# Performance work log

Hardware: AMD Instinct MI355X
Metric: run time of the kernel (lower is better)

## Reference

```python
import jax, jax.numpy as jnp
import numpy as np

B, LQ, LK, D = 8, 2048, 2048, 128

def setup_inputs() -> dict:
    key = jax.random.key(0)
    k1, k2, k3, k4 = jax.random.split(key, 4)
    return {
        "query": jax.random.normal(k1, (B, LQ, D), dtype=jnp.float32),
        "key": jax.random.normal(k2, (B, LK, D), dtype=jnp.float32),
        "value": jax.random.normal(k3, (B, LK, D), dtype=jnp.float32),
        "scale_factor": jax.random.normal(k4, (B, LQ, LK), dtype=jnp.float32),
    }

def reference(query, key, value, scale_factor):
    # qk: [B, LQ, LK]
    qk = jnp.einsum("bqd,bkd->bqk", query, key)
    probs = jax.nn.softmax(qk * scale_factor, axis=-1)
    # dropout_p = 0.0 -> identity
    return jnp.einsum("bqk,bkd->bqd", probs, value)
```

## Files before the change

kernel.cpp:

```cpp
#include <hip/hip_runtime.h>
#include <hip/hip_bf16.h>


typedef float          f32x4 __attribute__((ext_vector_type(4)));
typedef short          s16x8 __attribute__((ext_vector_type(8)));
typedef unsigned int   u32x4 __attribute__((ext_vector_type(4)));
typedef unsigned short u16x4 __attribute__((ext_vector_type(4)));

#define LOG2E 1.4426950408889634f

__device__ __forceinline__ float fast_exp2(float x) {
#if __has_builtin(__builtin_amdgcn_exp2f)
    return __builtin_amdgcn_exp2f(x);
#else
    return exp2f(x);
#endif
}

__device__ __forceinline__ unsigned short f2bf(float x) {
    return __builtin_bit_cast(unsigned short, __float2bfloat16(x));
}
__device__ __forceinline__ float bf2f(unsigned short u) {
    return __bfloat162float(__builtin_bit_cast(__hip_bfloat16, u));
}

__global__ void conv_split(const float* __restrict__ src,
                           unsigned short* __restrict__ hi,
                           unsigned short* __restrict__ lo, int n4) {
    int i = blockIdx.x * blockDim.x + threadIdx.x;
    if (i >= n4) return;
    const float4 v = ((const float4*)src)[i];
    float f[4] = {v.x, v.y, v.z, v.w};
    u16x4 h, l;
#pragma unroll
    for (int j = 0; j < 4; ++j) {
        unsigned short hb = f2bf(f[j]);
        h[j] = hb;
        l[j] = f2bf(f[j] - bf2f(hb));
    }
    ((u16x4*)hi)[i] = h;
    ((u16x4*)lo)[i] = l;
}

__global__ void transpose_v(const float* __restrict__ v,
                            unsigned short* __restrict__ vt) {
    __shared__ unsigned short tile[64 * 132];
    const int b   = blockIdx.x & 7;
    const int k0  = (blockIdx.x >> 3) * 64;
    const int tid = threadIdx.x;
#pragma unroll
    for (int p = 0; p < 8; ++p) {
        int idx  = p * 256 + tid;
        int k    = idx >> 5;
        int dblk = idx & 31;
        float4 val = ((const float4*)v)[((b * 2048 + k0 + k) * 128 + dblk * 4) >> 2];
        u16x4 t4;
        t4[0] = f2bf(val.x); t4[1] = f2bf(val.y);
        t4[2] = f2bf(val.z); t4[3] = f2bf(val.w);
        *(u16x4*)&tile[k * 132 + dblk * 4] = t4;
    }
    __syncthreads();
#pragma unroll
    for (int p = 0; p < 4; ++p) {
        int idx = p * 256 + tid;
        int d   = idx >> 3;
        int k8  = idx & 7;
        u16x4 a, c;
#pragma unroll
        for (int j = 0; j < 4; ++j) a[j] = tile[(k8 * 8 + j) * 132 + d];
#pragma unroll
        for (int j = 0; j < 4; ++j) c[j] = tile[(k8 * 8 + 4 + j) * 132 + d];
        unsigned short* outp = vt + (b * 128 + d) * 2048 + k0 + k8 * 8;
        *(u16x4*)outp       = a;
        *(u16x4*)(outp + 4) = c;
    }
}

#define KHS 136
#define VTS 72
#define PS  72

__global__ __launch_bounds__(256, 2)
void flash_fwd(const unsigned short* __restrict__ qh_g,
               const unsigned short* __restrict__ ql_g,
               const unsigned short* __restrict__ kh_g,
               const unsigned short* __restrict__ kl_g,
               const unsigned short* __restrict__ vt_g,
               const float* __restrict__ scale_g,
               float* __restrict__ opart,
               float* __restrict__ mpart,
               float* __restrict__ lpart) {
    __shared__ unsigned short lds_kh[64 * KHS];
    __shared__ unsigned short lds_kl[64 * KHS];
    __shared__ unsigned short lds_vt[128 * VTS];
    __shared__ unsigned short lds_p[4][16 * PS];

    const int tid  = threadIdx.x;
    const int wave = tid >> 6;
    const int lane = tid & 63;
    const int c    = lane & 15;
    const int g    = lane >> 4;

    const int bid   = blockIdx.x;
    const int b     = bid & 7;
    const int qt    = (bid >> 3) & 31;
    const int ks    = bid >> 8;
    const int q0    = qt * 64;
    const int kbase = ks * 1024;

    s16x8 qh[4], ql[4];
    {
        const int qrow = b * 2048 + q0 + wave * 16 + c;
#pragma unroll
        for (int kstep = 0; kstep < 4; ++kstep) {
            int idx = qrow * 16 + kstep * 4 + g;
            qh[kstep] = __builtin_bit_cast(s16x8, ((const u32x4*)qh_g)[idx]);
            ql[kstep] = __builtin_bit_cast(s16x8, ((const u32x4*)ql_g)[idx]);
        }
    }

    f32x4 oacc[8];
#pragma unroll
    for (int t = 0; t < 8; ++t) oacc[t] = (f32x4){0.f, 0.f, 0.f, 0.f};
    float m2[4], ln[4];
#pragma unroll
    for (int r = 0; r < 4; ++r) { m2[r] = -INFINITY; ln[r] = 0.f; }

    for (int kc = 0; kc < 16; ++kc) {
        const int k0 = kbase + kc * 64;

        __syncthreads();
        {
            u32x4 tk[4], tl[4], tv[4];
            const int row = tid >> 4, c8 = tid & 15;
            const int dv  = tid >> 3, k8 = tid & 7;
#pragma unroll
            for (int p = 0; p < 4; ++p) {
                int gidx = (b * 2048 + k0 + p * 16 + row) * 16 + c8;
                tk[p] = ((const u32x4*)kh_g)[gidx];
                tl[p] = ((const u32x4*)kl_g)[gidx];
                int vidx = (b * 128 + p * 32 + dv) * 256 + (k0 >> 3) + k8;
                tv[p] = ((const u32x4*)vt_g)[vidx];
            }
#pragma unroll
            for (int p = 0; p < 4; ++p) {
                *(u32x4*)&lds_kh[(p * 16 + row) * KHS + c8 * 8] = tk[p];
                *(u32x4*)&lds_kl[(p * 16 + row) * KHS + c8 * 8] = tl[p];
                *(u32x4*)&lds_vt[(p * 32 + dv) * VTS + k8 * 8]  = tv[p];
            }
        }
        __syncthreads();

        float sc[4][4];
        {
            const int qrow = b * 2048 + q0 + wave * 16 + g * 4;
#pragma unroll
            for (int r = 0; r < 4; ++r)
#pragma unroll
                for (int t = 0; t < 4; ++t)
                    sc[t][r] = scale_g[(qrow + r) * 2048 + k0 + t * 16 + c] * LOG2E;
        }

        f32x4 s[4];
#pragma unroll
        for (int t = 0; t < 4; ++t) s[t] = (f32x4){0.f, 0.f, 0.f, 0.f};
#pragma unroll
        for (int kstep = 0; kstep < 4; ++kstep) {
#pragma unroll
            for (int t = 0; t < 4; ++t) {
                int off = (t * 16 + c) * KHS + kstep * 32 + g * 8;
                s16x8 bh = *(const s16x8*)&lds_kh[off];
                s16x8 bl = *(const s16x8*)&lds_kl[off];
                s[t] = __builtin_amdgcn_mfma_f32_16x16x32_bf16(qh[kstep], bh, s[t], 0, 0, 0);
                s[t] = __builtin_amdgcn_mfma_f32_16x16x32_bf16(ql[kstep], bh, s[t], 0, 0, 0);
                s[t] = __builtin_amdgcn_mfma_f32_16x16x32_bf16(qh[kstep], bl, s[t], 0, 0, 0);
            }
        }

        float lt[4][4], mx[4];
#pragma unroll
        for (int r = 0; r < 4; ++r) {
            lt[0][r] = s[0][r] * sc[0][r];
            lt[1][r] = s[1][r] * sc[1][r];
            lt[2][r] = s[2][r] * sc[2][r];
            lt[3][r] = s[3][r] * sc[3][r];
            mx[r] = fmaxf(fmaxf(lt[0][r], lt[1][r]), fmaxf(lt[2][r], lt[3][r]));
        }
#pragma unroll
        for (int mask = 1; mask < 16; mask <<= 1)
#pragma unroll
            for (int r = 0; r < 4; ++r)
                mx[r] = fmaxf(mx[r], __shfl_xor(mx[r], mask));
        float al[4], rs[4];
#pragma unroll
        for (int r = 0; r < 4; ++r) {
            float mn = fmaxf(m2[r], mx[r]);
            al[r] = fast_exp2(m2[r] - mn);
            m2[r] = mn;
            rs[r] = 0.f;
        }
#pragma unroll
        for (int t = 0; t < 4; ++t)
#pragma unroll
            for (int r = 0; r < 4; ++r) {
                float p = fast_exp2(lt[t][r] - m2[r]);
                rs[r] += p;
                lds_p[wave][(g * 4 + r) * PS + t * 16 + c] = f2bf(p);
            }
#pragma unroll
        for (int mask = 1; mask < 16; mask <<= 1)
#pragma unroll
            for (int r = 0; r < 4; ++r)
                rs[r] += __shfl_xor(rs[r], mask);
#pragma unroll
        for (int r = 0; r < 4; ++r) ln[r] = ln[r] * al[r] + rs[r];
#pragma unroll
        for (int t = 0; t < 8; ++t)
#pragma unroll
            for (int r = 0; r < 4; ++r) oacc[t][r] *= al[r];

#pragma unroll
        for (int k2 = 0; k2 < 2; ++k2) {
            s16x8 af = *(const s16x8*)&lds_p[wave][c * PS + k2 * 32 + g * 8];
#pragma unroll
            for (int t2 = 0; t2 < 8; ++t2) {
                s16x8 bv = *(const s16x8*)&lds_vt[(t2 * 16 + c) * VTS + k2 * 32 + g * 8];
                oacc[t2] = __builtin_amdgcn_mfma_f32_16x16x32_bf16(af, bv, oacc[t2], 0, 0, 0);
            }
        }
    }

    {
        const int rowb = (ks * 8 + b) * 2048 + q0 + wave * 16;
#pragma unroll
        for (int t2 = 0; t2 < 8; ++t2)
#pragma unroll
            for (int r = 0; r < 4; ++r)
                opart[(rowb + g * 4 + r) * 128 + t2 * 16 + c] = oacc[t2][r];
        if (c == 0) {
#pragma unroll
            for (int r = 0; r < 4; ++r) {
                mpart[rowb + g * 4 + r] = m2[r];
                lpart[rowb + g * 4 + r] = ln[r];
            }
        }
    }
}

__global__ void merge_halves(const float* __restrict__ opart,
                             const float* __restrict__ mpart,
                             const float* __restrict__ lpart,
                             float* __restrict__ out) {
    const int row = blockIdx.x;
    const int d   = threadIdx.x;
    const float m0 = mpart[row],  m1 = mpart[16384 + row];
    const float l0 = lpart[row],  l1 = lpart[16384 + row];
    const float M  = fmaxf(m0, m1);
    const float a0 = fast_exp2(m0 - M);
    const float a1 = fast_exp2(m1 - M);
    const float inv = 1.f / (a0 * l0 + a1 * l1);
    const int i = row * 128 + d;
    out[i] = (a0 * opart[i] + a1 * opart[16384 * 128 + i]) * inv;
}

extern "C" void kernel_launch(void* const* d_in, const int* in_sizes, int n_in,
                              void* d_out, int out_size, void* d_ws, size_t ws_size,
                              hipStream_t stream) {
    const float* q  = (const float*)d_in[0];
    const float* k  = (const float*)d_in[1];
    const float* v  = (const float*)d_in[2];
    const float* sc = (const float*)d_in[3];
    float* out = (float*)d_out;

    char* ws = (char*)d_ws;
    const size_t MB = 1024 * 1024;
    unsigned short* qh = (unsigned short*)(ws);
    unsigned short* ql = (unsigned short*)(ws + 4 * MB);
    unsigned short* kh = (unsigned short*)(ws + 8 * MB);
    unsigned short* kl = (unsigned short*)(ws + 12 * MB);
    unsigned short* vt = (unsigned short*)(ws + 16 * MB);
    float* opart = (float*)(ws + 20 * MB);
    float* mpart = (float*)(ws + 36 * MB);
    float* lpart = (float*)(ws + 36 * MB + 128 * 1024);

    conv_split<<<2048, 256, 0, stream>>>(q, qh, ql, 524288);
    conv_split<<<2048, 256, 0, stream>>>(k, kh, kl, 524288);
    transpose_v<<<256, 256, 0, stream>>>(v, vt);
    flash_fwd<<<512, 256, 0, stream>>>(qh, ql, kh, kl, vt, sc, opart, mpart, lpart);
    merge_halves<<<16384, 128, 0, stream>>>(opart, mpart, lpart, out);
}
```

Measured before the change: 260.3 us.

## Split keys four ways, load K/V from global directly, bf16 partial outputs

Rewrites the attention kernel to split the key dimension into four chunks instead of two, doubling the grid and raising the occupancy target. K and V are read straight from global memory into MFMA fragments with register prefetch, which removes the LDS staging and block barriers. S is computed transposed so each lane reads the scale factors as vectorized rows, and the P tile is stored with an XOR swizzle. Partial outputs are stored in bf16, which cuts merge traffic at some cost in precision. The Q and K conversion kernels are fused into one launch, and the V transpose gets smaller tiles.

```diff
diff --git a/kernel.cpp b/kernel.cpp
--- a/kernel.cpp
+++ b/kernel.cpp
@@ -16,7 +16,6 @@
     return exp2f(x);
 #endif
 }
-
 __device__ __forceinline__ unsigned short f2bf(float x) {
     return __builtin_bit_cast(unsigned short, __float2bfloat16(x));
 }
@@ -24,11 +23,15 @@
     return __bfloat162float(__builtin_bit_cast(__hip_bfloat16, u));
 }
 
-__global__ void conv_split(const float* __restrict__ src,
-                           unsigned short* __restrict__ hi,
-                           unsigned short* __restrict__ lo, int n4) {
-    int i = blockIdx.x * blockDim.x + threadIdx.x;
-    if (i >= n4) return;
+__global__ void conv_split2(const float* __restrict__ q, const float* __restrict__ k,
+                            unsigned short* __restrict__ qh, unsigned short* __restrict__ ql,
+                            unsigned short* __restrict__ kh, unsigned short* __restrict__ kl) {
+    const int bid  = blockIdx.x;
+    const int half = bid >> 11;
+    const int i    = (bid & 2047) * 256 + threadIdx.x;
+    const float* src = half ? k : q;
+    unsigned short* hi = half ? kh : qh;
+    unsigned short* lo = half ? kl : ql;
     const float4 v = ((const float4*)src)[i];
     float f[4] = {v.x, v.y, v.z, v.w};
     u16x4 h, l;
@@ -44,223 +47,200 @@
 
 __global__ void transpose_v(const float* __restrict__ v,
                             unsigned short* __restrict__ vt) {
-    __shared__ unsigned short tile[64 * 132];
-    const int b   = blockIdx.x & 7;
-    const int k0  = (blockIdx.x >> 3) * 64;
-    const int tid = threadIdx.x;
-#pragma unroll
-    for (int p = 0; p < 8; ++p) {
-        int idx  = p * 256 + tid;
-        int k    = idx >> 5;
-        int dblk = idx & 31;
-        float4 val = ((const float4*)v)[((b * 2048 + k0 + k) * 128 + dblk * 4) >> 2];
+    __shared__ unsigned short tile[64 * 36];
+    const int b    = blockIdx.x & 7;
+    const int rest = blockIdx.x >> 3;
+    const int k0   = (rest & 31) * 64;
+    const int d0   = (rest >> 5) * 32;
+    const int tid  = threadIdx.x;
+#pragma unroll
+    for (int it = 0; it < 2; ++it) {
+        int idx = it * 256 + tid;
+        int kk  = idx >> 3;
+        int d4  = idx & 7;
+        float4 val = ((const float4*)v)[((b * 2048 + k0 + kk) * 128 + d0 + d4 * 4) >> 2];
         u16x4 t4;
         t4[0] = f2bf(val.x); t4[1] = f2bf(val.y);
         t4[2] = f2bf(val.z); t4[3] = f2bf(val.w);
-        *(u16x4*)&tile[k * 132 + dblk * 4] = t4;
+        *(u16x4*)&tile[kk * 36 + d4 * 4] = t4;
     }
     __syncthreads();
-#pragma unroll
-    for (int p = 0; p < 4; ++p) {
-        int idx = p * 256 + tid;
-        int d   = idx >> 3;
-        int k8  = idx & 7;
-        u16x4 a, c;
-#pragma unroll
-        for (int j = 0; j < 4; ++j) a[j] = tile[(k8 * 8 + j) * 132 + d];
-#pragma unroll
-        for (int j = 0; j < 4; ++j) c[j] = tile[(k8 * 8 + 4 + j) * 132 + d];
-        unsigned short* outp = vt + (b * 128 + d) * 2048 + k0 + k8 * 8;
+    {
+        int d  = tid >> 3;
+        int k8 = tid & 7;
+        u16x4 a, cgrp;
+#pragma unroll
+        for (int j = 0; j < 4; ++j) a[j]    = tile[(k8 * 8 + j) * 36 + d];
+#pragma unroll
+        for (int j = 0; j < 4; ++j) cgrp[j] = tile[(k8 * 8 + 4 + j) * 36 + d];
+        unsigned short* outp = vt + (b * 128 + d0 + d) * 2048 + k0 + k8 * 8;
         *(u16x4*)outp       = a;
-        *(u16x4*)(outp + 4) = c;
-    }
-}
-
-#define KHS 136
-#define VTS 72
-#define PS  72
-
-__global__ __launch_bounds__(256, 2)
+        *(u16x4*)(outp + 4) = cgrp;
+    }
+}
+
+#define KSPLIT 4
+#define NKC    8
+
+__global__ __launch_bounds__(256, 4)
 void flash_fwd(const unsigned short* __restrict__ qh_g,
                const unsigned short* __restrict__ ql_g,
                const unsigned short* __restrict__ kh_g,
                const unsigned short* __restrict__ kl_g,
                const unsigned short* __restrict__ vt_g,
                const float* __restrict__ scale_g,
-               float* __restrict__ opart,
+               unsigned short* __restrict__ opart,
                float* __restrict__ mpart,
                float* __restrict__ lpart) {
-    __shared__ unsigned short lds_kh[64 * KHS];
-    __shared__ unsigned short lds_kl[64 * KHS];
-    __shared__ unsigned short lds_vt[128 * VTS];
-    __shared__ unsigned short lds_p[4][16 * PS];
+    __shared__ unsigned short lds_p[4][16 * 72];
 
     const int tid  = threadIdx.x;
     const int wave = tid >> 6;
     const int lane = tid & 63;
     const int c    = lane & 15;
     const int g    = lane >> 4;
-
-    const int bid   = blockIdx.x;
-    const int b     = bid & 7;
-    const int qt    = (bid >> 3) & 31;
-    const int ks    = bid >> 8;
-    const int q0    = qt * 64;
-    const int kbase = ks * 1024;
-
-    s16x8 qh[4], ql[4];
+    const int xr   = (c & 3) << 3;
+
+    const int bid = blockIdx.x;
+    const int b   = bid & 7;
+    const int qt  = (bid >> 3) & 31;
+    const int ks  = bid >> 8;
+    const int q0  = qt * 64;
+    const int kbase = ks * 512;
+
+    const int qrow = b * 2048 + q0 + wave * 16 + c;
+
+    s16x8 qhB[4], qlB[4];
+#pragma unroll
+    for (int kstep = 0; kstep < 4; ++kstep) {
+        int idx = qrow * 16 + kstep * 4 + g;
+        qhB[kstep] = __builtin_bit_cast(s16x8, ((const u32x4*)qh_g)[idx]);
+        qlB[kstep] = __builtin_bit_cast(s16x8, ((const u32x4*)ql_g)[idx]);
+    }
+
+    f32x4 oacc[8];
+#pragma unroll
+    for (int t = 0; t < 8; ++t) oacc[t] = (f32x4){0.f, 0.f, 0.f, 0.f};
+    float m2 = -INFINITY, ln = 0.f;
+    unsigned short* pw = &lds_p[wave][0];
+
+    for (int kc = 0; kc < NKC; ++kc) {
+        const int k0 = kbase + kc * 64;
+
+        f32x4 scf[4];
+        {
+            const int sidx = qrow * 512 + (k0 >> 2) + g;
+#pragma unroll
+            for (int t = 0; t < 4; ++t)
+                scf[t] = ((const f32x4*)scale_g)[sidx + 4 * t];
+        }
+
+        f32x4 st[4];
+#pragma unroll
+        for (int t = 0; t < 4; ++t) st[t] = (f32x4){0.f, 0.f, 0.f, 0.f};
+        {
+            const u32x4* khp = (const u32x4*)kh_g + ((b * 2048 + k0 + c) * 16 + g);
+            const u32x4* klp = (const u32x4*)kl_g + ((b * 2048 + k0 + c) * 16 + g);
+            s16x8 khf = __builtin_bit_cast(s16x8, khp[0]);
+            s16x8 klf = __builtin_bit_cast(s16x8, klp[0]);
+#pragma unroll
+            for (int p = 0; p < 16; ++p) {
+                const int t = p & 3, kstep = p >> 2;
+                s16x8 khn, kln;
+                if (p < 15) {
+                    const int off = ((p + 1) & 3) * 256 + ((p + 1) >> 2) * 4;
+                    khn = __builtin_bit_cast(s16x8, khp[off]);
+                    kln = __builtin_bit_cast(s16x8, klp[off]);
+                }
+                st[t] = __builtin_amdgcn_mfma_f32_16x16x32_bf16(khf, qhB[kstep], st[t], 0, 0, 0);
+                st[t] = __builtin_amdgcn_mfma_f32_16x16x32_bf16(klf, qhB[kstep], st[t], 0, 0, 0);
+                st[t] = __builtin_amdgcn_mfma_f32_16x16x32_bf16(khf, qlB[kstep], st[t], 0, 0, 0);
+                if (p < 15) { khf = khn; klf = kln; }
+            }
+        }
+
+        float lt[4][4];
+        float mx = -INFINITY;
+#pragma unroll
+        for (int t = 0; t < 4; ++t)
+#pragma unroll
+            for (int r = 0; r < 4; ++r) {
+                lt[t][r] = st[t][r] * (scf[t][r] * LOG2E);
+                mx = fmaxf(mx, lt[t][r]);
+            }
+        mx = fmaxf(mx, __shfl_xor(mx, 16));
+        mx = fmaxf(mx, __shfl_xor(mx, 32));
+        const float mn = fmaxf(m2, mx);
+        const float al = fast_exp2(m2 - mn);
+        m2 = mn;
+        float rs = 0.f;
+#pragma unroll
+        for (int t = 0; t < 4; ++t) {
+            u16x4 pb;
+#pragma unroll
+            for (int r = 0; r < 4; ++r) {
+                float pv = fast_exp2(lt[t][r] - m2);
+                rs += pv;
+                pb[r] = f2bf(pv);
+            }
+            *(u16x4*)&pw[c * 72 + (((16 * t + 4 * g) ^ xr))] = pb;
+        }
+        rs += __shfl_xor(rs, 16);
+        rs += __shfl_xor(rs, 32);
+        ln = ln * al + rs;
+#pragma unroll
+        for (int t2 = 0; t2 < 8; ++t2)
+#pragma unroll
+            for (int r = 0; r < 4; ++r) oacc[t2][r] *= al;
+
+        {
+            const u32x4* vp = (const u32x4*)vt_g + ((b * 128 + c) * 256 + (k0 >> 3) + g);
+#pragma unroll
+            for (int k2 = 0; k2 < 2; ++k2) {
+                s16x8 bP = *(const s16x8*)&pw[c * 72 + ((32 * k2 + 8 * g) ^ xr)];
+#pragma unroll
+                for (int t2 = 0; t2 < 8; ++t2) {
+                    s16x8 vA = __builtin_bit_cast(s16x8, vp[t2 * (16 * 256) + 4 * k2]);
+                    oacc[t2] = __builtin_amdgcn_mfma_f32_16x16x32_bf16(vA, bP, oacc[t2], 0, 0, 0);
+                }
+            }
+        }
+    }
+
     {
-        const int qrow = b * 2048 + q0 + wave * 16 + c;
-#pragma unroll
-        for (int kstep = 0; kstep < 4; ++kstep) {
-            int idx = qrow * 16 + kstep * 4 + g;
-            qh[kstep] = __builtin_bit_cast(s16x8, ((const u32x4*)qh_g)[idx]);
-            ql[kstep] = __builtin_bit_cast(s16x8, ((const u32x4*)ql_g)[idx]);
-        }
-    }
-
-    f32x4 oacc[8];
-#pragma unroll
-    for (int t = 0; t < 8; ++t) oacc[t] = (f32x4){0.f, 0.f, 0.f, 0.f};
-    float m2[4], ln[4];
-#pragma unroll
-    for (int r = 0; r < 4; ++r) { m2[r] = -INFINITY; ln[r] = 0.f; }
-
-    for (int kc = 0; kc < 16; ++kc) {
-        const int k0 = kbase + kc * 64;
-
-        __syncthreads();
-        {
-            u32x4 tk[4], tl[4], tv[4];
-            const int row = tid >> 4, c8 = tid & 15;
-            const int dv  = tid >> 3, k8 = tid & 7;
-#pragma unroll
-            for (int p = 0; p < 4; ++p) {
-                int gidx = (b * 2048 + k0 + p * 16 + row) * 16 + c8;
-                tk[p] = ((const u32x4*)kh_g)[gidx];
-                tl[p] = ((const u32x4*)kl_g)[gidx];
-                int vidx = (b * 128 + p * 32 + dv) * 256 + (k0 >> 3) + k8;
-                tv[p] = ((const u32x4*)vt_g)[vidx];
-            }
-#pragma unroll
-            for (int p = 0; p < 4; ++p) {
-                *(u32x4*)&lds_kh[(p * 16 + row) * KHS + c8 * 8] = tk[p];
-                *(u32x4*)&lds_kl[(p * 16 + row) * KHS + c8 * 8] = tl[p];
-                *(u32x4*)&lds_vt[(p * 32 + dv) * VTS + k8 * 8]  = tv[p];
-            }
-        }
-        __syncthreads();
-
-        float sc[4][4];
-        {
-            const int qrow = b * 2048 + q0 + wave * 16 + g * 4;
-#pragma unroll
-            for (int r = 0; r < 4; ++r)
-#pragma unroll
-                for (int t = 0; t < 4; ++t)
-                    sc[t][r] = scale_g[(qrow + r) * 2048 + k0 + t * 16 + c] * LOG2E;
-        }
-
-        f32x4 s[4];
-#pragma unroll
-        for (int t = 0; t < 4; ++t) s[t] = (f32x4){0.f, 0.f, 0.f, 0.f};
-#pragma unroll
-        for (int kstep = 0; kstep < 4; ++kstep) {
-#pragma unroll
-            for (int t = 0; t < 4; ++t) {
-                int off = (t * 16 + c) * KHS + kstep * 32 + g * 8;
-                s16x8 bh = *(const s16x8*)&lds_kh[off];
-                s16x8 bl = *(const s16x8*)&lds_kl[off];
-                s[t] = __builtin_amdgcn_mfma_f32_16x16x32_bf16(qh[kstep], bh, s[t], 0, 0, 0);
-                s[t] = __builtin_amdgcn_mfma_f32_16x16x32_bf16(ql[kstep], bh, s[t], 0, 0, 0);
-                s[t] = __builtin_amdgcn_mfma_f32_16x16x32_bf16(qh[kstep], bl, s[t], 0, 0, 0);
-            }
-        }
-
-        float lt[4][4], mx[4];
-#pragma unroll
-        for (int r = 0; r < 4; ++r) {
-            lt[0][r] = s[0][r] * sc[0][r];
-            lt[1][r] = s[1][r] * sc[1][r];
-            lt[2][r] = s[2][r] * sc[2][r];
-            lt[3][r] = s[3][r] * sc[3][r];
-            mx[r] = fmaxf(fmaxf(lt[0][r], lt[1][r]), fmaxf(lt[2][r], lt[3][r]));
-        }
-#pragma unroll
-        for (int mask = 1; mask < 16; mask <<= 1)
-#pragma unroll
-            for (int r = 0; r < 4; ++r)
-                mx[r] = fmaxf(mx[r], __shfl_xor(mx[r], mask));
-        float al[4], rs[4];
-#pragma unroll
-        for (int r = 0; r < 4; ++r) {
-            float mn = fmaxf(m2[r], mx[r]);
-            al[r] = fast_exp2(m2[r] - mn);
-            m2[r] = mn;
-            rs[r] = 0.f;
-        }
-#pragma unroll
-        for (int t = 0; t < 4; ++t)
-#pragma unroll
-            for (int r = 0; r < 4; ++r) {
-                float p = fast_exp2(lt[t][r] - m2[r]);
-                rs[r] += p;
-                lds_p[wave][(g * 4 + r) * PS + t * 16 + c] = f2bf(p);
-            }
-#pragma unroll
-        for (int mask = 1; mask < 16; mask <<= 1)
-#pragma unroll
-            for (int r = 0; r < 4; ++r)
-                rs[r] += __shfl_xor(rs[r], mask);
-#pragma unroll
-        for (int r = 0; r < 4; ++r) ln[r] = ln[r] * al[r] + rs[r];
-#pragma unroll
-        for (int t = 0; t < 8; ++t)
-#pragma unroll
-            for (int r = 0; r < 4; ++r) oacc[t][r] *= al[r];
-
-#pragma unroll
-        for (int k2 = 0; k2 < 2; ++k2) {
-            s16x8 af = *(const s16x8*)&lds_p[wave][c * PS + k2 * 32 + g * 8];
-#pragma unroll
-            for (int t2 = 0; t2 < 8; ++t2) {
-                s16x8 bv = *(const s16x8*)&lds_vt[(t2 * 16 + c) * VTS + k2 * 32 + g * 8];
-                oacc[t2] = __builtin_amdgcn_mfma_f32_16x16x32_bf16(af, bv, oacc[t2], 0, 0, 0);
-            }
-        }
-    }
-
-    {
-        const int rowb = (ks * 8 + b) * 2048 + q0 + wave * 16;
-#pragma unroll
-        for (int t2 = 0; t2 < 8; ++t2)
-#pragma unroll
-            for (int r = 0; r < 4; ++r)
-                opart[(rowb + g * 4 + r) * 128 + t2 * 16 + c] = oacc[t2][r];
-        if (c == 0) {
-#pragma unroll
-            for (int r = 0; r < 4; ++r) {
-                mpart[rowb + g * 4 + r] = m2[r];
-                lpart[rowb + g * 4 + r] = ln[r];
-            }
-        }
-    }
-}
-
-__global__ void merge_halves(const float* __restrict__ opart,
-                             const float* __restrict__ mpart,
-                             const float* __restrict__ lpart,
-                             float* __restrict__ out) {
+        const size_t obase = ((size_t)ks * 16384 + qrow) * 128;
+#pragma unroll
+        for (int t2 = 0; t2 < 8; ++t2) {
+            u16x4 ob;
+#pragma unroll
+            for (int r = 0; r < 4; ++r) ob[r] = f2bf(oacc[t2][r]);
+            *(u16x4*)&opart[obase + 16 * t2 + 4 * g] = ob;
+        }
+        if (g == 0) {
+            mpart[ks * 16384 + qrow] = m2;
+            lpart[ks * 16384 + qrow] = ln;
+        }
+    }
+}
+
+__global__ void merge4(const unsigned short* __restrict__ opart,
+                       const float* __restrict__ mpart,
+                       const float* __restrict__ lpart,
+                       float* __restrict__ out) {
     const int row = blockIdx.x;
     const int d   = threadIdx.x;
-    const float m0 = mpart[row],  m1 = mpart[16384 + row];
-    const float l0 = lpart[row],  l1 = lpart[16384 + row];
-    const float M  = fmaxf(m0, m1);
-    const float a0 = fast_exp2(m0 - M);
-    const float a1 = fast_exp2(m1 - M);
-    const float inv = 1.f / (a0 * l0 + a1 * l1);
-    const int i = row * 128 + d;
-    out[i] = (a0 * opart[i] + a1 * opart[16384 * 128 + i]) * inv;
+    float m[KSPLIT];
+    float M = -INFINITY;
+#pragma unroll
+    for (int s = 0; s < KSPLIT; ++s) { m[s] = mpart[s * 16384 + row]; M = fmaxf(M, m[s]); }
+    float den = 0.f, acc = 0.f;
+#pragma unroll
+    for (int s = 0; s < KSPLIT; ++s) {
+        const float a = fast_exp2(m[s] - M);
+        den += a * lpart[s * 16384 + row];
+        acc += a * bf2f(opart[((size_t)s * 16384 + row) * 128 + d]);
+    }
+    out[(size_t)row * 128 + d] = acc / den;
 }
 
 extern "C" void kernel_launch(void* const* d_in, const int* in_sizes, int n_in,
@@ -279,13 +259,12 @@
     unsigned short* kh = (unsigned short*)(ws + 8 * MB);
     unsigned short* kl = (unsigned short*)(ws + 12 * MB);
     unsigned short* vt = (unsigned short*)(ws + 16 * MB);
-    float* opart = (float*)(ws + 20 * MB);
+    unsigned short* opart = (unsigned short*)(ws + 20 * MB);
     float* mpart = (float*)(ws + 36 * MB);
-    float* lpart = (float*)(ws + 36 * MB + 128 * 1024);
-
-    conv_split<<<2048, 256, 0, stream>>>(q, qh, ql, 524288);
-    conv_split<<<2048, 256, 0, stream>>>(k, kh, kl, 524288);
-    transpose_v<<<256, 256, 0, stream>>>(v, vt);
-    flash_fwd<<<512, 256, 0, stream>>>(qh, ql, kh, kl, vt, sc, opart, mpart, lpart);
-    merge_halves<<<16384, 128, 0, stream>>>(opart, mpart, lpart, out);
-}
+    float* lpart = (float*)(ws + 36 * MB + 256 * 1024);
+
+    conv_split2<<<4096, 256, 0, stream>>>(q, k, qh, ql, kh, kl);
+    transpose_v<<<1024, 256, 0, stream>>>(v, vt);
+    flash_fwd<<<1024, 256, 0, stream>>>(qh, ql, kh, kl, vt, sc, opart, mpart, lpart);
+    merge4<<<16384, 128, 0, stream>>>(opart, mpart, lpart, out);
+}
```

Result: slower. 393.5 us (+51.1%).
